# Kernel tuning notes

Hardware: AMD Instinct MI355X
Metric: run time of the kernel (lower is better)

The kernel has to match this reference:

```python
import jax, jax.numpy as jnp
import numpy as np

TOP_K = 2


def setup_inputs() -> dict:
    key = jax.random.key(0)
    ks = jax.random.split(key, 5)
    B, S, D, E, I = 1, 2048, 2880, 8, 2880
    scale_in = 1.0 / np.sqrt(D)
    scale_mid = 1.0 / np.sqrt(I)
    return {
        "x": jax.random.normal(ks[0], (B, S, D), dtype=jnp.float32),
        "w_router": jax.random.normal(ks[1], (D, E), dtype=jnp.float32) * scale_in,
        "w_gate": jax.random.normal(ks[2], (E, D, I), dtype=jnp.float32) * scale_in,
        "w_up": jax.random.normal(ks[3], (E, D, I), dtype=jnp.float32) * scale_in,
        "w_down": jax.random.normal(ks[4], (E, I, D), dtype=jnp.float32) * scale_mid,
    }


def reference(x, w_router, w_gate, w_up, w_down):
    B, S, D = x.shape
    E = w_router.shape[1]
    t = x.reshape(-1, D)  # [T, D] flattened tokens

    # --- RouterTopK: softmax over experts, then top-k selection ---
    logits = t @ w_router                      # [T, E]
    affinities = jax.nn.softmax(logits, axis=-1)
    top_vals, top_idx = jax.lax.top_k(affinities, TOP_K)   # [T, K]
    # normalize_top_k_affinities=True: renormalize selected weights to sum to 1
    top_vals = top_vals / jnp.sum(top_vals, axis=-1, keepdims=True)

    # scatter normalized weights into dense [T, E] combine matrix
    T = t.shape[0]
    tok = jnp.arange(T)[:, None]
    weights = jnp.zeros((T, E), dtype=t.dtype).at[tok, top_idx].set(top_vals)

    # --- Expert SiLU-GLU MLPs (computed per expert, combined by weights) ---
    gate = jnp.einsum("td,edi->eti", t, w_gate)  # [E, T, I]
    up = jnp.einsum("td,edi->eti", t, w_up)      # [E, T, I]
    h = jax.nn.silu(gate) * up                   # [E, T, I]
    y = jnp.einsum("eti,eid->etd", h, w_down)    # [E, T, D]

    out = jnp.einsum("te,etd->td", weights, y)   # affinity-weighted combine
    return out.reshape(B, S, D)
```

## Files before the change

### kernel.cpp

```cpp
#include <hip/hip_runtime.h>
#include <hip/hip_fp16.h>
#include <stdint.h>
#include <math.h>


typedef _Float16 f16;
typedef _Float16 f16x8 __attribute__((ext_vector_type(8)));
typedef float f32x4 __attribute__((ext_vector_type(4)));

#define T_TOK 2048
#define DDIM 2880
#define NEXP 8
#define IDIM 2880

#define BM 256
#define BK 64
#define NKT 45
#define BN1 96
#define NNT1 30
#define BN2 192
#define NNT2 15
#define MAXMT 24
#define NB1 (NNT1*MAXMT)
#define NB2 (NNT2*MAXMT)
#define SLOT_CAP 6144

#define HBUF_OFF 0
#define HBUF_BYTES ((size_t)SLOT_CAP*IDIM*2)
#define XH_OFF   (HBUF_OFF + HBUF_BYTES)
#define XH_BYTES ((size_t)T_TOK*DDIM*2)
#define YBUF_OFF XH_OFF
#define YBUF_BYTES ((size_t)SLOT_CAP*DDIM*2)
#define META_OFF (YBUF_OFF + YBUF_BYTES)
#define M_COUNT 0
#define M_CUR 8
#define M_OFFS 16
#define M_NTILES 25
#define M_TILE_E 32
#define M_TILE_R0 96
#define M_SLOT_TOK 160
#define M_SLOT_OF (160+SLOT_CAP)
#define M_TOK_E (M_SLOT_OF + 2*T_TOK)
#define META_INTS (M_TOK_E + 2*T_TOK)
#define SLOTW_OFF (META_OFF + META_INTS*4)
#define TOKW_OFF  (SLOTW_OFF + SLOT_CAP*4)
#define WS_NEEDED ((size_t)TOKW_OFF + (size_t)T_TOK*2*4)

__device__ __forceinline__ int swz(int row) { return ((row ^ (row >> 3)) & 7) << 4; }

__device__ __forceinline__ void gload_lds16(const void* gp, void* lp) {
  __builtin_amdgcn_global_load_lds(
      (const __attribute__((address_space(1))) uint32_t*)gp,
      (__attribute__((address_space(3))) uint32_t*)lp,
      16, 0, 0);
}

__global__ __launch_bounds__(256) void k_router(
    const float* __restrict__ x, const float* __restrict__ wr,
    int* __restrict__ meta, float* __restrict__ tok_w) {
  const int lane = threadIdx.x & 63;
  const int t = blockIdx.x * 4 + (threadIdx.x >> 6);
  double acc[NEXP];
#pragma unroll
  for (int e = 0; e < NEXP; e++) acc[e] = 0.0;
  for (int d = lane; d < DDIM; d += 64) {
    float xv = x[(size_t)t * DDIM + d];
    float4 w0 = *(const float4*)(wr + (size_t)d * NEXP);
    float4 w1 = *(const float4*)(wr + (size_t)d * NEXP + 4);
    acc[0] += (double)xv * (double)w0.x;
    acc[1] += (double)xv * (double)w0.y;
    acc[2] += (double)xv * (double)w0.z;
    acc[3] += (double)xv * (double)w0.w;
    acc[4] += (double)xv * (double)w1.x;
    acc[5] += (double)xv * (double)w1.y;
    acc[6] += (double)xv * (double)w1.z;
    acc[7] += (double)xv * (double)w1.w;
  }
#pragma unroll
  for (int m = 32; m >= 1; m >>= 1) {
#pragma unroll
    for (int e = 0; e < NEXP; e++) acc[e] += __shfl_xor(acc[e], m, 64);
  }
  if (lane == 0) {
    int e0 = 0;
#pragma unroll
    for (int e = 1; e < NEXP; e++) if (acc[e] > acc[e0]) e0 = e;
    int e1 = (e0 == 0) ? 1 : 0;
#pragma unroll
    for (int e = 0; e < NEXP; e++) if (e != e0 && acc[e] > acc[e1]) e1 = e;
    double w0 = 1.0 / (1.0 + exp(acc[e1] - acc[e0]));
    meta[M_TOK_E + 2*t]     = e0;
    meta[M_TOK_E + 2*t + 1] = e1;
    tok_w[2*t]     = (float)w0;
    tok_w[2*t + 1] = (float)(1.0 - w0);
    atomicAdd(&meta[M_COUNT + e0], 1);
    atomicAdd(&meta[M_COUNT + e1], 1);
  }
}

__global__ __launch_bounds__(256) void k_xcvt(const float* __restrict__ x, f16* __restrict__ xh) {
  size_t i = ((size_t)blockIdx.x * 256 + threadIdx.x) * 8;
  float4 a = *(const float4*)(x + i);
  float4 b = *(const float4*)(x + i + 4);
  f16x8 v;
  v[0]=(f16)a.x; v[1]=(f16)a.y; v[2]=(f16)a.z; v[3]=(f16)a.w;
  v[4]=(f16)b.x; v[5]=(f16)b.y; v[6]=(f16)b.z; v[7]=(f16)b.w;
  *(f16x8*)(xh + i) = v;
}

__global__ __launch_bounds__(64) void k_scan(int* __restrict__ meta, float* __restrict__ slot_w) {
  __shared__ int s_off[NEXP], s_cnt[NEXP], s_pc[NEXP];
  if (threadIdx.x == 0) {
    int run = 0, nt = 0;
    for (int e = 0; e < NEXP; e++) {
      int c = meta[M_COUNT + e];
      int mt = (c + BM - 1) / BM;
      meta[M_OFFS + e] = run;
      s_off[e] = run; s_cnt[e] = c; s_pc[e] = mt * BM;
      for (int j = 0; j < mt; j++) { meta[M_TILE_E + nt] = e; meta[M_TILE_R0 + nt] = run + j * BM; nt++; }
      run += mt * BM;
      meta[M_CUR + e] = 0;
    }
    meta[M_OFFS + NEXP] = run;
    meta[M_NTILES] = nt;
  }
  __syncthreads();
  for (int e = 0; e < NEXP; e++) {
    for (int i = s_cnt[e] + (int)threadIdx.x; i < s_pc[e]; i += 64) {
      meta[M_SLOT_TOK + s_off[e] + i] = 0;
      slot_w[s_off[e] + i] = 0.0f;
    }
  }
}

__global__ __launch_bounds__(256) void k_scatter(int* __restrict__ meta,
    float* __restrict__ slot_w, const float* __restrict__ tok_w) {
  int t = blockIdx.x * 256 + threadIdx.x;
  if (t >= T_TOK) return;
#pragma unroll
  for (int k = 0; k < 2; k++) {
    int e = meta[M_TOK_E + 2*t + k];
    int pos = atomicAdd(&meta[M_CUR + e], 1);
    int slot = meta[M_OFFS + e] + pos;
    meta[M_SLOT_TOK + slot] = t;
    slot_w[slot] = tok_w[2*t + k];
    meta[M_SLOT_OF + 2*t + k] = slot;
  }
}

__global__ __launch_bounds__(512, 2) void k_gemm1(
    const f16* __restrict__ xh, const float* __restrict__ wg, const float* __restrict__ wu,
    f16* __restrict__ hbuf, const int* __restrict__ meta) {
  const int id = blockIdx.x;
  const int sid = (id & 7) * (NB1 / 8) + (id >> 3);
  const int mt = sid % MAXMT;
  const int nb = sid / MAXMT;
  if (mt >= meta[M_NTILES]) return;
  const int e  = meta[M_TILE_E + mt];
  const int r0 = meta[M_TILE_R0 + mt];
  const int n0 = nb * BN1;

  __shared__ ushort sA[2][BM * BK];
  __shared__ ushort sB[2][BN1 * BK];

  const int tid  = threadIdx.x;
  const int lane = tid & 63;
  const int w    = tid >> 6;
  const int wm   = w >> 1;
  const int gu   = w & 1;

  const char* a_gbase[4];
  int a_loff[4];
#pragma unroll
  for (int i = 0; i < 4; i++) {
    int seg = w * 4 + i;
    int row = seg * 8 + (lane >> 3);
    int colb = ((lane & 7) * 16) ^ swz(row);
    int tok = meta[M_SLOT_TOK + r0 + row];
    a_gbase[i] = (const char*)(xh + (size_t)tok * DDIM) + colb;
    a_loff[i] = seg * 1024;
  }

  const int bm_ = tid / 192;
  const int tt  = tid % 192;
  const int bn0 = (tt % 24) * 4;
  const int bk0 = (tt / 24) * 8;
  const bool bact = tid < 384;
  const float* bsrc = (bm_ ? wu : wg) + ((size_t)e * DDIM + bk0) * IDIM + n0 + bn0;

  float4 vB[8];
  f32x4 acc[4][6];
#pragma unroll
  for (int i = 0; i < 4; i++)
#pragma unroll
    for (int j = 0; j < 6; j++) acc[i][j] = {0.f,0.f,0.f,0.f};

#pragma unroll
  for (int i = 0; i < 4; i++) gload_lds16(a_gbase[i], (char*)sA[0] + a_loff[i]);
  if (bact) {
#pragma unroll
    for (int j = 0; j < 8; j++) vB[j] = *(const float4*)(bsrc + (size_t)j * IDIM);
  }

  for (int kt = 0; kt < NKT; kt++) {
    const int cur = kt & 1;
    __syncthreads();
    if (bact) {
#pragma unroll
      for (int c = 0; c < 4; c++) {
        f16x8 p;
#pragma unroll
        for (int j = 0; j < 8; j++) {
          float fc = (c==0) ? vB[j].x : (c==1) ? vB[j].y : (c==2) ? vB[j].z : vB[j].w;
          p[j] = (f16)fc;
        }
        *(f16x8*)((char*)sB[bm_] + (bn0 + c) * 128 + ((bk0 * 2) ^ swz(bn0 + c))) = p;
      }
    }
    __syncthreads();
    if (kt + 1 < NKT) {
#pragma unroll
      for (int i = 0; i < 4; i++)
        gload_lds16(a_gbase[i] + (kt + 1) * 128, (char*)sA[cur ^ 1] + a_loff[i]);
      if (bact) {
        const float* bs = bsrc + (size_t)(kt + 1) * BK * IDIM;
#pragma unroll
        for (int j = 0; j < 8; j++) vB[j] = *(const float4*)(bs + (size_t)j * IDIM);
      }
    }
#pragma unroll
    for (int kk = 0; kk < 2; kk++) {
      const int gb = kk * 64 + ((lane >> 4) * 16);
      f16x8 af[4], bf[6];
#pragma unroll
      for (int fm = 0; fm < 4; fm++) {
        int row = wm * 64 + fm * 16 + (lane & 15);
        af[fm] = *(const f16x8*)((const char*)sA[cur] + row * 128 + (gb ^ swz(row)));
      }
#pragma unroll
      for (int fn = 0; fn < 6; fn++) {
        int row = fn * 16 + (lane & 15);
        bf[fn] = *(const f16x8*)((const char*)sB[gu] + row * 128 + (gb ^ swz(row)));
      }
#pragma unroll
      for (int fm = 0; fm < 4; fm++)
#pragma unroll
        for (int fn = 0; fn < 6; fn++)
          acc[fm][fn] = __builtin_amdgcn_mfma_f32_16x16x32_f16(af[fm], bf[fn], acc[fm][fn], 0, 0, 0);
    }
  }

  float* u_lds = (float*)&sA[0][0];
  const int rl4 = (lane >> 4) * 4;
  const int cl  = lane & 15;
#pragma unroll
  for (int r = 0; r < 2; r++) {
    __syncthreads();
    if (gu == 1) {
#pragma unroll
      for (int fi = 0; fi < 2; fi++)
#pragma unroll
        for (int fn = 0; fn < 6; fn++)
#pragma unroll
          for (int j = 0; j < 4; j++)
            u_lds[wm * 3200 + (fi * 16 + rl4 + j) * 100 + fn * 16 + cl] = acc[2*r + fi][fn][j];
    }
    __syncthreads();
    if (gu == 0) {
#pragma unroll
      for (int fi = 0; fi < 2; fi++) {
        int fm = 2*r + fi;
#pragma unroll
        for (int fn = 0; fn < 6; fn++)
#pragma unroll
          for (int j = 0; j < 4; j++) {
            float u = u_lds[wm * 3200 + (fi * 16 + rl4 + j) * 100 + fn * 16 + cl];
            float g = acc[fm][fn][j];
            float h = g * u / (1.0f + __expf(-g));
            hbuf[(size_t)(r0 + wm * 64 + fm * 16 + rl4 + j) * IDIM + n0 + fn * 16 + cl] = (f16)h;
          }
      }
    }
  }
}

__global__ __launch_bounds__(512, 2) void k_gemm2(
    const f16* __restrict__ hbuf, const float* __restrict__ wd,
    f16* __restrict__ ybuf, const int* __restrict__ meta, const float* __restrict__ slot_w) {
  const int id = blockIdx.x;
  const int sid = (id & 7) * (NB2 / 8) + (id >> 3);
  const int mt = sid % MAXMT;
  const int nb = sid / MAXMT;
  if (mt >= meta[M_NTILES]) return;
  const int e  = meta[M_TILE_E + mt];
  const int r0 = meta[M_TILE_R0 + mt];
  const int n0 = nb * BN2;

  __shared__ ushort sA[2][BM * BK];
  __shared__ ushort sB1[BN2 * BK];

  const int tid  = threadIdx.x;
  const int lane = tid & 63;
  const int w    = tid >> 6;
  const int wm   = w >> 1;
  const int wn   = w & 1;

  const char* a_gbase[4];
  int a_loff[4];
#pragma unroll
  for (int i = 0; i < 4; i++) {
    int seg = w * 4 + i;
    int row = seg * 8 + (lane >> 3);
    int colb = ((lane & 7) * 16) ^ swz(row);
    a_gbase[i] = (const char*)(hbuf + (size_t)(r0 + row) * IDIM) + colb;
    a_loff[i] = seg * 1024;
  }

  const int half = tid / 192;
  const int tt   = tid % 192;
  const int bn0  = half * 96 + (tt % 24) * 4;
  const int bk0  = (tt / 24) * 8;
  const bool bact = tid < 384;
  const float* bsrc = wd + ((size_t)e * IDIM + bk0) * DDIM + n0 + bn0;

  float4 vB[8];
  f32x4 acc[4][6];
#pragma unroll
  for (int i = 0; i < 4; i++)
#pragma unroll
    for (int j = 0; j < 6; j++) acc[i][j] = {0.f,0.f,0.f,0.f};

#pragma unroll
  for (int i = 0; i < 4; i++) gload_lds16(a_gbase[i], (char*)sA[0] + a_loff[i]);
  if (bact) {
#pragma unroll
    for (int j = 0; j < 8; j++) vB[j] = *(const float4*)(bsrc + (size_t)j * DDIM);
  }

  for (int kt = 0; kt < NKT; kt++) {
    const int cur = kt & 1;
    __syncthreads();
    if (bact) {
#pragma unroll
      for (int c = 0; c < 4; c++) {
        f16x8 p;
#pragma unroll
        for (int j = 0; j < 8; j++) {
          float fc = (c==0) ? vB[j].x : (c==1) ? vB[j].y : (c==2) ? vB[j].z : vB[j].w;
          p[j] = (f16)fc;
        }
        *(f16x8*)((char*)sB1 + (bn0 + c) * 128 + ((bk0 * 2) ^ swz(bn0 + c))) = p;
      }
    }
    __syncthreads();
    if (kt + 1 < NKT) {
#pragma unroll
      for (int i = 0; i < 4; i++)
        gload_lds16(a_gbase[i] + (kt + 1) * 128, (char*)sA[cur ^ 1] + a_loff[i]);
      if (bact) {
        const float* bs = bsrc + (size_t)(kt + 1) * BK * DDIM;
#pragma unroll
        for (int j = 0; j < 8; j++) vB[j] = *(const float4*)(bs + (size_t)j * DDIM);
      }
    }
#pragma unroll
    for (int kk = 0; kk < 2; kk++) {
      const int gb = kk * 64 + ((lane >> 4) * 16);
      f16x8 af[4], bf[6];
#pragma unroll
      for (int fm = 0; fm < 4; fm++) {
        int row = wm * 64 + fm * 16 + (lane & 15);
        af[fm] = *(const f16x8*)((const char*)sA[cur] + row * 128 + (gb ^ swz(row)));
      }
#pragma unroll
      for (int fn = 0; fn < 6; fn++) {
        int row = wn * 96 + fn * 16 + (lane & 15);
        bf[fn] = *(const f16x8*)((const char*)sB1 + row * 128 + (gb ^ swz(row)));
      }
#pragma unroll
      for (int fm = 0; fm < 4; fm++)
#pragma unroll
        for (int fn = 0; fn < 6; fn++)
          acc[fm][fn] = __builtin_amdgcn_mfma_f32_16x16x32_f16(af[fm], bf[fn], acc[fm][fn], 0, 0, 0);
    }
  }

  const int rl4 = (lane >> 4) * 4;
  const int cl  = lane & 15;
#pragma unroll
  for (int fm = 0; fm < 4; fm++)
#pragma unroll
    for (int j = 0; j < 4; j++) {
      int row = wm * 64 + fm * 16 + rl4 + j;
      int slot = r0 + row;
      float wv = slot_w[slot];
#pragma unroll
      for (int fn = 0; fn < 6; fn++) {
        int col = n0 + wn * 96 + fn * 16 + cl;
        ybuf[(size_t)slot * DDIM + col] = (f16)(acc[fm][fn][j] * wv);
      }
    }
}

__global__ __launch_bounds__(256) void k_combine(const f16* __restrict__ ybuf,
    const int* __restrict__ meta, float* __restrict__ out) {
  size_t idx = (size_t)blockIdx.x * 256 + threadIdx.x;
  int t = (int)(idx / (DDIM/8));
  int c = (int)(idx % (DDIM/8));
  int s0 = meta[M_SLOT_OF + 2*t];
  int s1 = meta[M_SLOT_OF + 2*t + 1];
  f16x8 a = *(const f16x8*)(ybuf + (size_t)s0 * DDIM + c*8);
  f16x8 b = *(const f16x8*)(ybuf + (size_t)s1 * DDIM + c*8);
  float4 o0, o1;
  o0.x = (float)a[0] + (float)b[0];
  o0.y = (float)a[1] + (float)b[1];
  o0.z = (float)a[2] + (float)b[2];
  o0.w = (float)a[3] + (float)b[3];
  o1.x = (float)a[4] + (float)b[4];
  o1.y = (float)a[5] + (float)b[5];
  o1.z = (float)a[6] + (float)b[6];
  o1.w = (float)a[7] + (float)b[7];
  float* op = out + (size_t)t * DDIM + c*8;
  *(float4*)op = o0;
  *(float4*)(op + 4) = o1;
}

extern "C" void kernel_launch(void* const* d_in, const int* in_sizes, int n_in,
                              void* d_out, int out_size, void* d_ws, size_t ws_size,
                              hipStream_t stream) {
  const float* x  = (const float*)d_in[0];
  const float* wr = (const float*)d_in[1];
  const float* wg = (const float*)d_in[2];
  const float* wu = (const float*)d_in[3];
  const float* wd = (const float*)d_in[4];
  float* out = (float*)d_out;
  char* ws = (char*)d_ws;
  if (ws_size < WS_NEEDED) return;

  f16* hbuf  = (f16*)(ws + HBUF_OFF);
  f16* xh    = (f16*)(ws + XH_OFF);
  f16* ybuf  = (f16*)(ws + YBUF_OFF);
  int* meta  = (int*)(ws + META_OFF);
  float* slot_w = (float*)(ws + SLOTW_OFF);
  float* tok_w  = (float*)(ws + TOKW_OFF);

  hipMemsetAsync(meta + M_COUNT, 0, NEXP * sizeof(int), stream);
  k_router<<<T_TOK/4, 256, 0, stream>>>(x, wr, meta, tok_w);
  k_xcvt<<<(T_TOK*DDIM/8 + 255)/256, 256, 0, stream>>>(x, xh);
  k_scan<<<1, 64, 0, stream>>>(meta, slot_w);
  k_scatter<<<(T_TOK + 255)/256, 256, 0, stream>>>(meta, slot_w, tok_w);
  k_gemm1<<<NB1, 512, 0, stream>>>(xh, wg, wu, hbuf, meta);
  k_gemm2<<<NB2, 512, 0, stream>>>(hbuf, wd, ybuf, meta, slot_w);
  k_combine<<<(T_TOK*DDIM/8 + 255)/256, 256, 0, stream>>>(ybuf, meta, out);
}
```

Measured before the change: 691.3 us.

## Double-buffer B tiles in LDS to use one barrier per k-step

Both expert GEMM kernels now keep two LDS buffers for the fp16-converted weight tile. The next tile's conversion and store happen after the MFMA work of the current step, into the other buffer. This cuts the loop to one __syncthreads per k-step instead of two and lets the MFMAs start without waiting on the conversion. In exchange LDS use per block goes up (sB doubles to about 48KB in gemm1 and sB1 to 48KB in gemm2), which could limit the 2-blocks-per-CU occupancy target.

After: 687.3 us. No clear change (-0.6%).

```diff
diff --git a/kernel.cpp b/kernel.cpp
--- a/kernel.cpp
+++ b/kernel.cpp
@@ -161,7 +161,7 @@
   const int n0 = nb * BN1;
 
   __shared__ ushort sA[2][BM * BK];
-  __shared__ ushort sB[2][BN1 * BK];
+  __shared__ ushort sB[2][2][BN1 * BK];
 
   const int tid  = threadIdx.x;
   const int lane = tid & 63;
@@ -200,12 +200,52 @@
   if (bact) {
 #pragma unroll
     for (int j = 0; j < 8; j++) vB[j] = *(const float4*)(bsrc + (size_t)j * IDIM);
-  }
+#pragma unroll
+    for (int c = 0; c < 4; c++) {
+      f16x8 p;
+#pragma unroll
+      for (int j = 0; j < 8; j++) {
+        float fc = (c==0) ? vB[j].x : (c==1) ? vB[j].y : (c==2) ? vB[j].z : vB[j].w;
+        p[j] = (f16)fc;
+      }
+      *(f16x8*)((char*)sB[0][bm_] + (bn0 + c) * 128 + ((bk0 * 2) ^ swz(bn0 + c))) = p;
+    }
+  }
+  __syncthreads();
 
   for (int kt = 0; kt < NKT; kt++) {
     const int cur = kt & 1;
-    __syncthreads();
-    if (bact) {
+    if (kt + 1 < NKT) {
+#pragma unroll
+      for (int i = 0; i < 4; i++)
+        gload_lds16(a_gbase[i] + (kt + 1) * 128, (char*)sA[cur ^ 1] + a_loff[i]);
+      if (bact) {
+        const float* bs = bsrc + (size_t)(kt + 1) * BK * IDIM;
+#pragma unroll
+        for (int j = 0; j < 8; j++) vB[j] = *(const float4*)(bs + (size_t)j * IDIM);
+      }
+    }
+#pragma unroll
+    for (int kk = 0; kk < 2; kk++) {
+      const int gb = kk * 64 + ((lane >> 4) * 16);
+      f16x8 af[4], bf[6];
+#pragma unroll
+      for (int fm = 0; fm < 4; fm++) {
+        int row = wm * 64 + fm * 16 + (lane & 15);
+        af[fm] = *(const f16x8*)((const char*)sA[cur] + row * 128 + (gb ^ swz(row)));
+      }
+#pragma unroll
+      for (int fn = 0; fn < 6; fn++) {
+        int row = fn * 16 + (lane & 15);
+        bf[fn] = *(const f16x8*)((const char*)sB[cur][gu] + row * 128 + (gb ^ swz(row)));
+      }
+#pragma unroll
+      for (int fm = 0; fm < 4; fm++)
+#pragma unroll
+        for (int fn = 0; fn < 6; fn++)
+          acc[fm][fn] = __builtin_amdgcn_mfma_f32_16x16x32_f16(af[fm], bf[fn], acc[fm][fn], 0, 0, 0);
+    }
+    if (kt + 1 < NKT && bact) {
 #pragma unroll
       for (int c = 0; c < 4; c++) {
         f16x8 p;
@@ -214,40 +254,10 @@
           float fc = (c==0) ? vB[j].x : (c==1) ? vB[j].y : (c==2) ? vB[j].z : vB[j].w;
           p[j] = (f16)fc;
         }
-        *(f16x8*)((char*)sB[bm_] + (bn0 + c) * 128 + ((bk0 * 2) ^ swz(bn0 + c))) = p;
+        *(f16x8*)((char*)sB[cur ^ 1][bm_] + (bn0 + c) * 128 + ((bk0 * 2) ^ swz(bn0 + c))) = p;
       }
     }
     __syncthreads();
-    if (kt + 1 < NKT) {
-#pragma unroll
-      for (int i = 0; i < 4; i++)
-        gload_lds16(a_gbase[i] + (kt + 1) * 128, (char*)sA[cur ^ 1] + a_loff[i]);
-      if (bact) {
-        const float* bs = bsrc + (size_t)(kt + 1) * BK * IDIM;
-#pragma unroll
-        for (int j = 0; j < 8; j++) vB[j] = *(const float4*)(bs + (size_t)j * IDIM);
-      }
-    }
-#pragma unroll
-    for (int kk = 0; kk < 2; kk++) {
-      const int gb = kk * 64 + ((lane >> 4) * 16);
-      f16x8 af[4], bf[6];
-#pragma unroll
-      for (int fm = 0; fm < 4; fm++) {
-        int row = wm * 64 + fm * 16 + (lane & 15);
-        af[fm] = *(const f16x8*)((const char*)sA[cur] + row * 128 + (gb ^ swz(row)));
-      }
-#pragma unroll
-      for (int fn = 0; fn < 6; fn++) {
-        int row = fn * 16 + (lane & 15);
-        bf[fn] = *(const f16x8*)((const char*)sB[gu] + row * 128 + (gb ^ swz(row)));
-      }
-#pragma unroll
-      for (int fm = 0; fm < 4; fm++)
-#pragma unroll
-        for (int fn = 0; fn < 6; fn++)
-          acc[fm][fn] = __builtin_amdgcn_mfma_f32_16x16x32_f16(af[fm], bf[fn], acc[fm][fn], 0, 0, 0);
-    }
   }
 
   float* u_lds = (float*)&sA[0][0];
@@ -297,7 +307,7 @@
   const int n0 = nb * BN2;
 
   __shared__ ushort sA[2][BM * BK];
-  __shared__ ushort sB1[BN2 * BK];
+  __shared__ ushort sB1[2][BN2 * BK];
 
   const int tid  = threadIdx.x;
   const int lane = tid & 63;
@@ -335,12 +345,52 @@
   if (bact) {
 #pragma unroll
     for (int j = 0; j < 8; j++) vB[j] = *(const float4*)(bsrc + (size_t)j * DDIM);
-  }
+#pragma unroll
+    for (int c = 0; c < 4; c++) {
+      f16x8 p;
+#pragma unroll
+      for (int j = 0; j < 8; j++) {
+        float fc = (c==0) ? vB[j].x : (c==1) ? vB[j].y : (c==2) ? vB[j].z : vB[j].w;
+        p[j] = (f16)fc;
+      }
+      *(f16x8*)((char*)sB1[0] + (bn0 + c) * 128 + ((bk0 * 2) ^ swz(bn0 + c))) = p;
+    }
+  }
+  __syncthreads();
 
   for (int kt = 0; kt < NKT; kt++) {
     const int cur = kt & 1;
-    __syncthreads();
-    if (bact) {
+    if (kt + 1 < NKT) {
+#pragma unroll
+      for (int i = 0; i < 4; i++)
+        gload_lds16(a_gbase[i] + (kt + 1) * 128, (char*)sA[cur ^ 1] + a_loff[i]);
+      if (bact) {
+        const float* bs = bsrc + (size_t)(kt + 1) * BK * DDIM;
+#pragma unroll
+        for (int j = 0; j < 8; j++) vB[j] = *(const float4*)(bs + (size_t)j * DDIM);
+      }
+    }
+#pragma unroll
+    for (int kk = 0; kk < 2; kk++) {
+      const int gb = kk * 64 + ((lane >> 4) * 16);
+      f16x8 af[4], bf[6];
+#pragma unroll
+      for (int fm = 0; fm < 4; fm++) {
+        int row = wm * 64 + fm * 16 + (lane & 15);
+        af[fm] = *(const f16x8*)((const char*)sA[cur] + row * 128 + (gb ^ swz(row)));
+      }
+#pragma unroll
+      for (int fn = 0; fn < 6; fn++) {
+        int row = wn * 96 + fn * 16 + (lane & 15);
+        bf[fn] = *(const f16x8*)((const char*)sB1[cur] + row * 128 + (gb ^ swz(row)));
+      }
+#pragma unroll
+      for (int fm = 0; fm < 4; fm++)
+#pragma unroll
+        for (int fn = 0; fn < 6; fn++)
+          acc[fm][fn] = __builtin_amdgcn_mfma_f32_16x16x32_f16(af[fm], bf[fn], acc[fm][fn], 0, 0, 0);
+    }
+    if (kt + 1 < NKT && bact) {
 #pragma unroll
       for (int c = 0; c < 4; c++) {
         f16x8 p;
@@ -349,40 +399,10 @@
           float fc = (c==0) ? vB[j].x : (c==1) ? vB[j].y : (c==2) ? vB[j].z : vB[j].w;
           p[j] = (f16)fc;
         }
-        *(f16x8*)((char*)sB1 + (bn0 + c) * 128 + ((bk0 * 2) ^ swz(bn0 + c))) = p;
+        *(f16x8*)((char*)sB1[cur ^ 1] + (bn0 + c) * 128 + ((bk0 * 2) ^ swz(bn0 + c))) = p;
       }
     }
     __syncthreads();
-    if (kt + 1 < NKT) {
-#pragma unroll
-      for (int i = 0; i < 4; i++)
-        gload_lds16(a_gbase[i] + (kt + 1) * 128, (char*)sA[cur ^ 1] + a_loff[i]);
-      if (bact) {
-        const float* bs = bsrc + (size_t)(kt + 1) * BK * DDIM;
-#pragma unroll
-        for (int j = 0; j < 8; j++) vB[j] = *(const float4*)(bs + (size_t)j * DDIM);
-      }
-    }
-#pragma unroll
-    for (int kk = 0; kk < 2; kk++) {
-      const int gb = kk * 64 + ((lane >> 4) * 16);
-      f16x8 af[4], bf[6];
-#pragma unroll
-      for (int fm = 0; fm < 4; fm++) {
-        int row = wm * 64 + fm * 16 + (lane & 15);
-        af[fm] = *(const f16x8*)((const char*)sA[cur] + row * 128 + (gb ^ swz(row)));
-      }
-#pragma unroll
-      for (int fn = 0; fn < 6; fn++) {
-        int row = wn * 96 + fn * 16 + (lane & 15);
-        bf[fn] = *(const f16x8*)((const char*)sB1 + row * 128 + (gb ^ swz(row)));
-      }
-#pragma unroll
-      for (int fm = 0; fm < 4; fm++)
-#pragma unroll
-        for (int fn = 0; fn < 6; fn++)
-          acc[fm][fn] = __builtin_amdgcn_mfma_f32_16x16x32_f16(af[fm], bf[fn], acc[fm][fn], 0, 0, 0);
-    }
   }
 
   const int rl4 = (lane >> 4) * 4;
```

## Double-buffer B tiles with two-stage register prefetch and single barrier per k-step

Applied to the files above, without the earlier changes.

Both expert GEMM kernels now double-buffer the converted fp16 weight tile in LDS and keep two register sets of fp32 weight loads in flight, prefetching two k-steps ahead. The two __syncthreads per iteration become one hand-written s_waitcnt/s_barrier placed after the MFMA block, so weight conversion overlaps compute. It also raises wave priority around the MFMA section. In exchange it doubles B LDS use, which may lower occupancy, and it depends on hand-counted vmcnt values that must match the compiler's actual load ordering.

Result: slower. 786.1 us (+13.7%).

```diff
diff --git a/kernel.cpp b/kernel.cpp
--- a/kernel.cpp
+++ b/kernel.cpp
@@ -55,6 +55,24 @@
       16, 0, 0);
 }
 
+__device__ __forceinline__ void ldB8(const float* bs, size_t stride, float4 (&v)[8]) {
+#pragma unroll
+  for (int j = 0; j < 8; j++) v[j] = *(const float4*)(bs + j * stride);
+}
+
+__device__ __forceinline__ void cvtB(const float4 (&v)[8], char* base, int bn0, int bk0) {
+#pragma unroll
+  for (int c = 0; c < 4; c++) {
+    f16x8 p;
+#pragma unroll
+    for (int j = 0; j < 8; j++) {
+      float fc = (c==0) ? v[j].x : (c==1) ? v[j].y : (c==2) ? v[j].z : v[j].w;
+      p[j] = (f16)fc;
+    }
+    *(f16x8*)(base + (bn0 + c) * 128 + ((bk0 * 2) ^ swz(bn0 + c))) = p;
+  }
+}
+
 __global__ __launch_bounds__(256) void k_router(
     const float* __restrict__ x, const float* __restrict__ wr,
     int* __restrict__ meta, float* __restrict__ tok_w) {
@@ -161,7 +179,7 @@
   const int n0 = nb * BN1;
 
   __shared__ ushort sA[2][BM * BK];
-  __shared__ ushort sB[2][BN1 * BK];
+  __shared__ ushort sB[2][2][BN1 * BK];
 
   const int tid  = threadIdx.x;
   const int lane = tid & 63;
@@ -188,7 +206,7 @@
   const bool bact = tid < 384;
   const float* bsrc = (bm_ ? wu : wg) + ((size_t)e * DDIM + bk0) * IDIM + n0 + bn0;
 
-  float4 vB[8];
+  float4 vB0[8], vB1[8];
   f32x4 acc[4][6];
 #pragma unroll
   for (int i = 0; i < 4; i++)
@@ -198,36 +216,28 @@
 #pragma unroll
   for (int i = 0; i < 4; i++) gload_lds16(a_gbase[i], (char*)sA[0] + a_loff[i]);
   if (bact) {
-#pragma unroll
-    for (int j = 0; j < 8; j++) vB[j] = *(const float4*)(bsrc + (size_t)j * IDIM);
+    ldB8(bsrc, IDIM, vB0);
+    asm volatile("s_waitcnt vmcnt(0)" ::: "memory");
+    cvtB(vB0, (char*)sB[0][bm_], bn0, bk0);
+    ldB8(bsrc + (size_t)BK * IDIM, IDIM, vB1);
+    asm volatile("s_waitcnt vmcnt(8) lgkmcnt(0)\n\ts_barrier" ::: "memory");
+  } else {
+    asm volatile("s_waitcnt vmcnt(0) lgkmcnt(0)\n\ts_barrier" ::: "memory");
   }
 
   for (int kt = 0; kt < NKT; kt++) {
     const int cur = kt & 1;
-    __syncthreads();
-    if (bact) {
-#pragma unroll
-      for (int c = 0; c < 4; c++) {
-        f16x8 p;
-#pragma unroll
-        for (int j = 0; j < 8; j++) {
-          float fc = (c==0) ? vB[j].x : (c==1) ? vB[j].y : (c==2) ? vB[j].z : vB[j].w;
-          p[j] = (f16)fc;
-        }
-        *(f16x8*)((char*)sB[bm_] + (bn0 + c) * 128 + ((bk0 * 2) ^ swz(bn0 + c))) = p;
-      }
-    }
-    __syncthreads();
-    if (kt + 1 < NKT) {
+    const bool nx1 = (kt + 1 < NKT), nx2 = (kt + 2 < NKT);
+    if (nx1) {
 #pragma unroll
       for (int i = 0; i < 4; i++)
         gload_lds16(a_gbase[i] + (kt + 1) * 128, (char*)sA[cur ^ 1] + a_loff[i]);
-      if (bact) {
-        const float* bs = bsrc + (size_t)(kt + 1) * BK * IDIM;
-#pragma unroll
-        for (int j = 0; j < 8; j++) vB[j] = *(const float4*)(bs + (size_t)j * IDIM);
-      }
-    }
+    }
+    if (nx2 && bact) {
+      const float* bs = bsrc + (size_t)(kt + 2) * BK * IDIM;
+      if (cur == 0) ldB8(bs, IDIM, vB0); else ldB8(bs, IDIM, vB1);
+    }
+    __builtin_amdgcn_s_setprio(1);
 #pragma unroll
     for (int kk = 0; kk < 2; kk++) {
       const int gb = kk * 64 + ((lane >> 4) * 16);
@@ -240,13 +250,24 @@
 #pragma unroll
       for (int fn = 0; fn < 6; fn++) {
         int row = fn * 16 + (lane & 15);
-        bf[fn] = *(const f16x8*)((const char*)sB[gu] + row * 128 + (gb ^ swz(row)));
+        bf[fn] = *(const f16x8*)((const char*)sB[cur][gu] + row * 128 + (gb ^ swz(row)));
       }
 #pragma unroll
       for (int fm = 0; fm < 4; fm++)
 #pragma unroll
         for (int fn = 0; fn < 6; fn++)
           acc[fm][fn] = __builtin_amdgcn_mfma_f32_16x16x32_f16(af[fm], bf[fn], acc[fm][fn], 0, 0, 0);
+    }
+    __builtin_amdgcn_s_setprio(0);
+    if (nx1 && bact) {
+      if (nx2) asm volatile("s_waitcnt vmcnt(12)" ::: "memory");
+      else     asm volatile("s_waitcnt vmcnt(4)" ::: "memory");
+      if (cur == 0) cvtB(vB1, (char*)sB[1][bm_], bn0, bk0);
+      else          cvtB(vB0, (char*)sB[0][bm_], bn0, bk0);
+    }
+    if (nx1) {
+      if (bact && nx2) asm volatile("s_waitcnt vmcnt(8) lgkmcnt(0)\n\ts_barrier" ::: "memory");
+      else             asm volatile("s_waitcnt vmcnt(0) lgkmcnt(0)\n\ts_barrier" ::: "memory");
     }
   }
 
@@ -297,7 +318,7 @@
   const int n0 = nb * BN2;
 
   __shared__ ushort sA[2][BM * BK];
-  __shared__ ushort sB1[BN2 * BK];
+  __shared__ ushort sB1[2][BN2 * BK];
 
   const int tid  = threadIdx.x;
   const int lane = tid & 63;
@@ -323,7 +344,7 @@
   const bool bact = tid < 384;
   const float* bsrc = wd + ((size_t)e * IDIM + bk0) * DDIM + n0 + bn0;
 
-  float4 vB[8];
+  float4 vB0[8], vB1[8];
   f32x4 acc[4][6];
 #pragma unroll
   for (int i = 0; i < 4; i++)
@@ -333,36 +354,28 @@
 #pragma unroll
   for (int i = 0; i < 4; i++) gload_lds16(a_gbase[i], (char*)sA[0] + a_loff[i]);
   if (bact) {
-#pragma unroll
-    for (int j = 0; j < 8; j++) vB[j] = *(const float4*)(bsrc + (size_t)j * DDIM);
+    ldB8(bsrc, DDIM, vB0);
+    asm volatile("s_waitcnt vmcnt(0)" ::: "memory");
+    cvtB(vB0, (char*)sB1[0], bn0, bk0);
+    ldB8(bsrc + (size_t)BK * DDIM, DDIM, vB1);
+    asm volatile("s_waitcnt vmcnt(8) lgkmcnt(0)\n\ts_barrier" ::: "memory");
+  } else {
+    asm volatile("s_waitcnt vmcnt(0) lgkmcnt(0)\n\ts_barrier" ::: "memory");
   }
 
   for (int kt = 0; kt < NKT; kt++) {
     const int cur = kt & 1;
-    __syncthreads();
-    if (bact) {
-#pragma unroll
-      for (int c = 0; c < 4; c++) {
-        f16x8 p;
-#pragma unroll
-        for (int j = 0; j < 8; j++) {
-          float fc = (c==0) ? vB[j].x : (c==1) ? vB[j].y : (c==2) ? vB[j].z : vB[j].w;
-          p[j] = (f16)fc;
-        }
-        *(f16x8*)((char*)sB1 + (bn0 + c) * 128 + ((bk0 * 2) ^ swz(bn0 + c))) = p;
-      }
-    }
-    __syncthreads();
-    if (kt + 1 < NKT) {
+    const bool nx1 = (kt + 1 < NKT), nx2 = (kt + 2 < NKT);
+    if (nx1) {
 #pragma unroll
       for (int i = 0; i < 4; i++)
         gload_lds16(a_gbase[i] + (kt + 1) * 128, (char*)sA[cur ^ 1] + a_loff[i]);
-      if (bact) {
-        const float* bs = bsrc + (size_t)(kt + 1) * BK * DDIM;
-#pragma unroll
-        for (int j = 0; j < 8; j++) vB[j] = *(const float4*)(bs + (size_t)j * DDIM);
-      }
-    }
+    }
+    if (nx2 && bact) {
+      const float* bs = bsrc + (size_t)(kt + 2) * BK * DDIM;
+      if (cur == 0) ldB8(bs, DDIM, vB0); else ldB8(bs, DDIM, vB1);
+    }
+    __builtin_amdgcn_s_setprio(1);
 #pragma unroll
     for (int kk = 0; kk < 2; kk++) {
       const int gb = kk * 64 + ((lane >> 4) * 16);
@@ -375,13 +388,24 @@
 #pragma unroll
       for (int fn = 0; fn < 6; fn++) {
         int row = wn * 96 + fn * 16 + (lane & 15);
-        bf[fn] = *(const f16x8*)((const char*)sB1 + row * 128 + (gb ^ swz(row)));
+        bf[fn] = *(const f16x8*)((const char*)sB1[cur] + row * 128 + (gb ^ swz(row)));
       }
 #pragma unroll
       for (int fm = 0; fm < 4; fm++)
 #pragma unroll
         for (int fn = 0; fn < 6; fn++)
           acc[fm][fn] = __builtin_amdgcn_mfma_f32_16x16x32_f16(af[fm], bf[fn], acc[fm][fn], 0, 0, 0);
+    }
+    __builtin_amdgcn_s_setprio(0);
+    if (nx1 && bact) {
+      if (nx2) asm volatile("s_waitcnt vmcnt(12)" ::: "memory");
+      else     asm volatile("s_waitcnt vmcnt(4)" ::: "memory");
+      if (cur == 0) cvtB(vB1, (char*)sB1[1], bn0, bk0);
+      else          cvtB(vB0, (char*)sB1[0], bn0, bk0);
+    }
+    if (nx1) {
+      if (bact && nx2) asm volatile("s_waitcnt vmcnt(8) lgkmcnt(0)\n\ts_barrier" ::: "memory");
+      else             asm volatile("s_waitcnt vmcnt(0) lgkmcnt(0)\n\ts_barrier" ::: "memory");
     }
   }
 
```
